# Optimization experiments

Measured on AMD Instinct MI355X. Metric: run time of the kernel, lower is better.

## Reference

```python
import jax, jax.numpy as jnp
import numpy as np

HEADS = 8
DIM_HEAD = 64


def setup_inputs() -> dict:
    key = jax.random.key(0)
    ks = jax.random.split(key, 4)
    B, C, H, W = 1, 256, 64, 64
    inner = HEADS * DIM_HEAD  # 512
    x = jax.random.normal(ks[0], (B, C, H, W), dtype=jnp.float32)
    norm_w = jnp.ones((C,), dtype=jnp.float32)                      # RMSNorm weight (1,C,1,1) flattened
    w_qkv = jax.random.normal(ks[1], (3 * inner, C), dtype=jnp.float32) * 0.02  # 1x1 conv, no bias
    w_out = jax.random.normal(ks[2], (C, inner), dtype=jnp.float32) * 0.02      # 1x1 conv
    b_out = jax.random.normal(ks[3], (C,), dtype=jnp.float32) * 0.02
    return {"x": x, "norm_w": norm_w, "w_qkv": w_qkv, "w_out": w_out, "b_out": b_out}


def reference(x, norm_w, w_qkv, w_out, b_out):
    B, C, H, W = x.shape
    N = H * W
    # RMSNorm: F.normalize over channel dim (L2, eps clamp) * weight * sqrt(C)
    l2 = jnp.sqrt(jnp.sum(x * x, axis=1, keepdims=True))
    xn = x / jnp.maximum(l2, 1e-12) * norm_w[None, :, None, None] * (C ** 0.5)
    # 1x1 conv QKV = channel matmul
    qkv = jnp.einsum('oc,bchw->bohw', w_qkv, xn)  # [B, 3*inner, H, W]
    q, k, v = jnp.split(qkv, 3, axis=1)

    def split_heads(t):
        # 'b (h d) x y -> b h (x y) d'
        return t.reshape(B, HEADS, DIM_HEAD, N).transpose(0, 1, 3, 2)

    q, k, v = map(split_heads, (q, k, v))
    scale = DIM_HEAD ** -0.5
    scores = jnp.einsum('bhnd,bhmd->bhnm', q, k) * scale  # [B,H,N,N]
    attn = jax.nn.softmax(scores, axis=-1)
    out = jnp.einsum('bhnm,bhmd->bhnd', attn, v)
    # 'b h (x y) d -> b (h d) x y'
    out = out.transpose(0, 1, 3, 2).reshape(B, HEADS * DIM_HEAD, H, W)
    # output 1x1 conv + residual (note: residual is the NORMALIZED x, per source)
    return jnp.einsum('ci,bihw->bchw', w_out, out) + b_out[None, :, None, None] + xn
```

## Files before the change

### kernel.cpp

```cpp
#include <hip/hip_runtime.h>


#define NPIX 4096
#define CIN 256
#define INNER 512
#define NHEAD 8
#define DH 64

typedef _Float16 f16;
typedef __attribute__((ext_vector_type(8))) _Float16 f16x8;
typedef __attribute__((ext_vector_type(4))) float f32x4;

static __device__ __forceinline__ f32x4 mfma_f16(f16x8 a, f16x8 b, f32x4 c) {
  return __builtin_amdgcn_mfma_f32_16x16x32_f16(a, b, c, 0, 0, 0);
}

static __device__ __forceinline__ unsigned pk2(float lo, float hi) {
  return __builtin_bit_cast(unsigned, __builtin_amdgcn_cvt_pkrtz(lo, hi));
}

__global__ __launch_bounds__(256) void k_cvt2(const float* __restrict__ a1, int n1,
                                              const float* __restrict__ a2, int n2,
                                              f16* __restrict__ b) {
  int i = blockIdx.x * 256 + threadIdx.x;
  if (i < n1) b[i] = (f16)a1[i];
  else if (i < n1 + n2) b[i] = (f16)a2[i - n1];
}

__global__ __launch_bounds__(256) void k_rmsnorm(const float* __restrict__ x,
                                                 const float* __restrict__ w,
                                                 float* __restrict__ xn,
                                                 f16* __restrict__ xnT) {
  const int pi = threadIdx.x & 15, cs = threadIdx.x >> 4;
  const int p = blockIdx.x * 16 + pi;
  __shared__ float red[16][16];
  float xv[16];
  float ss = 0.f;
#pragma unroll
  for (int i = 0; i < 16; ++i) {
    xv[i] = x[(cs * 16 + i) * NPIX + p];
    ss += xv[i] * xv[i];
  }
  red[cs][pi] = ss;
  __syncthreads();
  float tot = 0.f;
#pragma unroll
  for (int s = 0; s < 16; ++s) tot += red[s][pi];
  float inv = 16.0f / fmaxf(sqrtf(tot), 1e-12f);
  union { f16x8 v[2]; f16 h[16]; } hv;
#pragma unroll
  for (int i = 0; i < 16; ++i) {
    int c = cs * 16 + i;
    float v = xv[i] * inv * w[c];
    xn[c * NPIX + p] = v;
    hv.h[i] = (f16)v;
  }
  *(f16x8*)(xnT + (size_t)p * CIN + cs * 16) = hv.v[0];
  *(f16x8*)(xnT + (size_t)p * CIN + cs * 16 + 8) = hv.v[1];
}

__global__ __launch_bounds__(256) void k_qkv(const f16* __restrict__ wqkv,
                                             const f16* __restrict__ xnT,
                                             f16* __restrict__ qT,
                                             f16* __restrict__ kT,
                                             f16* __restrict__ vv) {
  const int lane = threadIdx.x & 63, wave = threadIdx.x >> 6;
  const int l15 = lane & 15, quad = lane >> 4;
  const int obase = blockIdx.y * 64 + (wave >> 1) * 32;
  const int pbase = blockIdx.x * 128 + (wave & 1) * 64;
  const int sect = blockIdx.y >> 3;
  f32x4 acc[8];
#pragma unroll
  for (int i = 0; i < 8; ++i) acc[i] = (f32x4){0.f, 0.f, 0.f, 0.f};
#pragma unroll
  for (int kc = 0; kc < CIN / 32; ++kc) {
    f16x8 af[2], bfr[4];
#pragma unroll
    for (int oc = 0; oc < 2; ++oc)
      af[oc] = *(const f16x8*)(wqkv + (size_t)(obase + oc * 16 + l15) * CIN + kc * 32 + quad * 8);
#pragma unroll
    for (int pc = 0; pc < 4; ++pc)
      bfr[pc] = *(const f16x8*)(xnT + (size_t)(pbase + pc * 16 + l15) * CIN + kc * 32 + quad * 8);
    if (sect < 2) {
#pragma unroll
      for (int pc = 0; pc < 4; ++pc)
#pragma unroll
        for (int oc = 0; oc < 2; ++oc)
          acc[pc * 2 + oc] = mfma_f16(bfr[pc], af[oc], acc[pc * 2 + oc]);
    } else {
#pragma unroll
      for (int oc = 0; oc < 2; ++oc)
#pragma unroll
        for (int pc = 0; pc < 4; ++pc)
          acc[oc * 4 + pc] = mfma_f16(af[oc], bfr[pc], acc[oc * 4 + pc]);
    }
  }
  if (sect < 2) {
    f16* dst = (sect == 0) ? qT : kT;
    const float sc = (sect == 0) ? 0.18033688f : 1.0f;
    const int head = blockIdx.y & 7;
    const int dd = (wave >> 1) * 32;
#pragma unroll
    for (int pc = 0; pc < 4; ++pc)
#pragma unroll
      for (int oc = 0; oc < 2; ++oc)
#pragma unroll
        for (int r = 0; r < 4; ++r) {
          int p = pbase + pc * 16 + quad * 4 + r;
          dst[((size_t)(head << 12) + p) * DH + dd + oc * 16 + l15] =
              (f16)(acc[pc * 2 + oc][r] * sc);
        }
  } else {
#pragma unroll
    for (int oc = 0; oc < 2; ++oc)
#pragma unroll
      for (int r = 0; r < 4; ++r) {
        int o = obase + oc * 16 + quad * 4 + r - 2 * INNER;
#pragma unroll
        for (int pc = 0; pc < 4; ++pc)
          vv[(size_t)o * NPIX + pbase + pc * 16 + l15] = (f16)acc[oc * 4 + pc][r];
      }
  }
}

__global__ __launch_bounds__(512, 2) void k_attn(const f16* __restrict__ qT,
                                                 const f16* __restrict__ kT,
                                                 const f16* __restrict__ vv,
                                                 f16* __restrict__ Ows) {
  const int head = blockIdx.x & 7;
  const int qb = (blockIdx.x >> 3) * 128;
  const int tid = threadIdx.x;
  const int wave = tid >> 6, lane = tid & 63;
  const int l15 = lane & 15, quad = lane >> 4;

  extern __shared__ float smem[];
  float (*Om)[4][64][17] = reinterpret_cast<float (*)[4][64][17]>(smem);
  float (*Ll)[4][16]     = reinterpret_cast<float (*)[4][16]>(smem + 8 * 4 * 64 * 17);

  f16x8 qf[8][2];
#pragma unroll
  for (int qt = 0; qt < 8; ++qt)
#pragma unroll
    for (int kc = 0; kc < 2; ++kc)
      qf[qt][kc] = *(const f16x8*)(qT + ((size_t)(head << 12) + qb + qt * 16 + l15) * DH + kc * 32 + quad * 8);

  f32x4 o[8][4];
  float ol[8];
#pragma unroll
  for (int qt = 0; qt < 8; ++qt) {
#pragma unroll
    for (int c = 0; c < 4; ++c) o[qt][c] = (f32x4){0.f, 0.f, 0.f, 0.f};
    ol[qt] = 0.f;
  }

  const f16* kbase = kT + (size_t)(head << 12) * DH;
  const f16* vbase = vv + (size_t)(head * DH) * NPIX;
  const int kb0 = wave * (NPIX / 8);
  const int srcA4 = (((quad & 1) << 5) + l15) * 4;
  const int srcB4 = srcA4 + 64;
  const bool hiQuad = quad >= 2;

  for (int it = 0; it < 16; ++it) {
    const int kb = kb0 + it * 32;
    f16x8 kf[2][2];
#pragma unroll
    for (int nc = 0; nc < 2; ++nc)
#pragma unroll
      for (int kc = 0; kc < 2; ++kc)
        kf[nc][kc] = *(const f16x8*)(kbase + (size_t)(kb + nc * 16 + l15) * DH + kc * 32 + quad * 8);
    f16x8 vf[4];
#pragma unroll
    for (int c = 0; c < 4; ++c)
      vf[c] = *(const f16x8*)(vbase + (size_t)(c * 16 + l15) * NPIX + kb + quad * 8);

#define S_QT(QT, S)                                                       \
  do {                                                                    \
    S[0] = mfma_f16(kf[0][0], qf[QT][0], (f32x4){0.f, 0.f, 0.f, 0.f});    \
    S[0] = mfma_f16(kf[0][1], qf[QT][1], S[0]);                           \
    S[1] = mfma_f16(kf[1][0], qf[QT][0], (f32x4){0.f, 0.f, 0.f, 0.f});    \
    S[1] = mfma_f16(kf[1][1], qf[QT][1], S[1]);                           \
  } while (0)

    f32x4 sc[2], sn[2];
    __builtin_amdgcn_s_setprio(1);
    S_QT(0, sc);
    __builtin_amdgcn_s_setprio(0);
#pragma unroll
    for (int qt = 0; qt < 8; ++qt) {
      if (qt < 7) {
        __builtin_amdgcn_s_setprio(1);
        S_QT(qt + 1, sn);
        __builtin_amdgcn_s_setprio(0);
      }
      float p0[4], p1[4];
#pragma unroll
      for (int r = 0; r < 4; ++r) {
        p0[r] = __builtin_amdgcn_exp2f(sc[0][r]);
        p1[r] = __builtin_amdgcn_exp2f(sc[1][r]);
      }
      ol[qt] += ((p0[0] + p0[1]) + (p0[2] + p0[3])) +
                ((p1[0] + p1[1]) + (p1[2] + p1[3]));
      unsigned A0 = pk2(p0[0], p0[1]), B0 = pk2(p0[2], p0[3]);
      unsigned A1 = pk2(p1[0], p1[1]), B1 = pk2(p1[2], p1[3]);
      unsigned As = hiQuad ? A1 : A0;
      unsigned Bs = hiQuad ? B1 : B0;
      union { f16x8 v; unsigned u[4]; } pf;
      pf.u[0] = (unsigned)__builtin_amdgcn_ds_bpermute(srcA4, (int)As);
      pf.u[1] = (unsigned)__builtin_amdgcn_ds_bpermute(srcA4, (int)Bs);
      pf.u[2] = (unsigned)__builtin_amdgcn_ds_bpermute(srcB4, (int)As);
      pf.u[3] = (unsigned)__builtin_amdgcn_ds_bpermute(srcB4, (int)Bs);
      __builtin_amdgcn_s_setprio(1);
#pragma unroll
      for (int c = 0; c < 4; ++c) o[qt][c] = mfma_f16(vf[c], pf.v, o[qt][c]);
      __builtin_amdgcn_s_setprio(0);
      if (qt < 7) { sc[0] = sn[0]; sc[1] = sn[1]; }
    }
#undef S_QT
  }

#pragma unroll
  for (int qt = 0; qt < 8; ++qt) {
    ol[qt] += __shfl_xor(ol[qt], 16);
    ol[qt] += __shfl_xor(ol[qt], 32);
  }

#pragma unroll
  for (int pass = 0; pass < 2; ++pass) {
    if (pass) __syncthreads();
#pragma unroll
    for (int qt2 = 0; qt2 < 4; ++qt2) {
      const int qt = pass * 4 + qt2;
      if (quad == 0) Ll[wave][qt2][l15] = ol[qt];
#pragma unroll
      for (int c = 0; c < 4; ++c)
#pragma unroll
        for (int r = 0; r < 4; ++r)
          Om[wave][qt2][c * 16 + quad * 4 + r][l15] = o[qt][c][r];
    }
    __syncthreads();
    const int d = tid & 63;
    const int mqt = wave >> 1, qh = (wave & 1) * 8;
#pragma unroll
    for (int j = 0; j < 8; ++j) {
      const int q = qh + j;
      float O = 0.f, L = 0.f;
#pragma unroll
      for (int w = 0; w < 8; ++w) {
        O += Om[w][mqt][d][q];
        L += Ll[w][mqt][q];
      }
      Ows[((size_t)(head << 12) + qb + (pass * 4 + mqt) * 16 + q) * DH + d] =
          (f16)(O / L);
    }
  }
}

__global__ __launch_bounds__(256) void k_oproj(const f16* __restrict__ wout,
                                               const f16* __restrict__ Ows,
                                               const float* __restrict__ bout,
                                               const float* __restrict__ xn,
                                               float* __restrict__ out) {
  const int lane = threadIdx.x & 63, wave = threadIdx.x >> 6;
  const int l15 = lane & 15, quad = lane >> 4;
  const int mbase = blockIdx.y * 32 + (wave >> 1) * 16;
  const int pbase = blockIdx.x * 64 + (wave & 1) * 32;
  f32x4 acc[2];
  acc[0] = (f32x4){0.f, 0.f, 0.f, 0.f};
  acc[1] = (f32x4){0.f, 0.f, 0.f, 0.f};
#pragma unroll
  for (int kc = 0; kc < INNER / 32; ++kc) {
    f16x8 af = *(const f16x8*)(wout + (size_t)(mbase + l15) * INNER + kc * 32 + quad * 8);
    int i0 = kc * 32 + quad * 8;
    int head = i0 >> 6, d0 = i0 & 63;
#pragma unroll
    for (int pc = 0; pc < 2; ++pc) {
      f16x8 bfr = *(const f16x8*)(Ows + ((size_t)(head << 12) + pbase + pc * 16 + l15) * DH + d0);
      acc[pc] = mfma_f16(af, bfr, acc[pc]);
    }
  }
#pragma unroll
  for (int pc = 0; pc < 2; ++pc)
#pragma unroll
    for (int r = 0; r < 4; ++r) {
      int c = mbase + quad * 4 + r, p = pbase + pc * 16 + l15;
      out[c * NPIX + p] = acc[pc][r] + bout[c] + xn[c * NPIX + p];
    }
}

extern "C" void kernel_launch(void* const* d_in, const int* in_sizes, int n_in,
                              void* d_out, int out_size, void* d_ws, size_t ws_size,
                              hipStream_t stream) {
  (void)in_sizes; (void)n_in; (void)out_size; (void)ws_size;
  const float* x      = (const float*)d_in[0];
  const float* norm_w = (const float*)d_in[1];
  const float* w_qkv  = (const float*)d_in[2];
  const float* w_out  = (const float*)d_in[3];
  const float* b_out  = (const float*)d_in[4];
  float* out = (float*)d_out;

  char* ws = (char*)d_ws;
  float* xn    = (float*)(ws);
  f16* xnT     = (f16*)(ws + (4u << 20));
  f16* qT      = (f16*)(ws + (6u << 20));
  f16* kT      = (f16*)(ws + (10u << 20));
  f16* vv      = (f16*)(ws + (14u << 20));
  f16* Ows     = (f16*)(ws + (18u << 20));
  f16* wqkv_h  = (f16*)(ws + (22u << 20));
  f16* wout_h  = (f16*)(ws + (22u << 20) + 786432);

  const int n1 = 3 * INNER * CIN, n2 = CIN * INNER;
  hipLaunchKernelGGL(k_cvt2, dim3((n1 + n2 + 255) / 256), dim3(256), 0, stream,
                     w_qkv, n1, w_out, n2, wqkv_h);
  hipLaunchKernelGGL(k_rmsnorm, dim3(NPIX / 16), dim3(256), 0, stream, x, norm_w, xn, xnT);
  hipLaunchKernelGGL(k_qkv, dim3(NPIX / 128, 1536 / 64), dim3(256), 0, stream,
                     wqkv_h, xnT, qT, kT, vv);
  hipLaunchKernelGGL(k_attn, dim3(256), dim3(512), 141312, stream,
                     qT, kT, vv, Ows);
  hipLaunchKernelGGL(k_oproj, dim3(NPIX / 64, CIN / 32), dim3(256), 0, stream,
                     wout_h, Ows, b_out, xn, out);
}
```

Measured before the change: 169.1 us.

## Split attention over keys with LDS-staged K/V tiles and a merge kernel

The attention kernel is restructured: each block now handles 128 queries for one head and one quarter of the keys. K/V tiles are double-buffered in LDS through direct global-to-LDS loads with XOR swizzling, so waves share them instead of each loading K/V from global memory. Partial outputs and row sums go to workspace and a new merge kernel combines them. This drops the large LDS cross-wave reduction and raises the block count for occupancy, at the cost of extra global traffic for the partials and one more launch.

New measurement: 154.8 us. -8.5%, faster.

```diff
diff --git a/kernel.cpp b/kernel.cpp
--- a/kernel.cpp
+++ b/kernel.cpp
@@ -17,6 +17,12 @@
 
 static __device__ __forceinline__ unsigned pk2(float lo, float hi) {
   return __builtin_bit_cast(unsigned, __builtin_amdgcn_cvt_pkrtz(lo, hi));
+}
+
+static __device__ __forceinline__ void gload_lds16(const void* g, void* l) {
+  __builtin_amdgcn_global_load_lds(
+      (const __attribute__((address_space(1))) unsigned*)g,
+      (__attribute__((address_space(3))) unsigned*)l, 16, 0, 0);
 }
 
 __global__ __launch_bounds__(256) void k_cvt2(const float* __restrict__ a1, int n1,
@@ -123,136 +129,171 @@
   }
 }
 
-__global__ __launch_bounds__(512, 2) void k_attn(const f16* __restrict__ qT,
+template <typename PT>
+__global__ __launch_bounds__(256, 4) void k_attn(const f16* __restrict__ qT,
                                                  const f16* __restrict__ kT,
                                                  const f16* __restrict__ vv,
-                                                 f16* __restrict__ Ows) {
-  const int head = blockIdx.x & 7;
-  const int qb = (blockIdx.x >> 3) * 128;
+                                                 PT* __restrict__ Opart,
+                                                 float* __restrict__ Lpart) {
+  const int bid = blockIdx.x;
+  const int head = bid & 7, split = (bid >> 3) & 3, qb = bid >> 5;
   const int tid = threadIdx.x;
   const int wave = tid >> 6, lane = tid & 63;
   const int l15 = lane & 15, quad = lane >> 4;
-
-  extern __shared__ float smem[];
-  float (*Om)[4][64][17] = reinterpret_cast<float (*)[4][64][17]>(smem);
-  float (*Ll)[4][16]     = reinterpret_cast<float (*)[4][16]>(smem + 8 * 4 * 64 * 17);
-
-  f16x8 qf[8][2];
-#pragma unroll
-  for (int qt = 0; qt < 8; ++qt)
+  const int keybase = split * 1024;
+
+  __shared__ f16 KV[2][8192];
+
+  const int qrow = (head << 12) + qb * 128 + wave * 32;
+  f16x8 qf[2][2];
+#pragma unroll
+  for (int qt = 0; qt < 2; ++qt)
 #pragma unroll
     for (int kc = 0; kc < 2; ++kc)
-      qf[qt][kc] = *(const f16x8*)(qT + ((size_t)(head << 12) + qb + qt * 16 + l15) * DH + kc * 32 + quad * 8);
-
-  f32x4 o[8][4];
-  float ol[8];
-#pragma unroll
-  for (int qt = 0; qt < 8; ++qt) {
+      qf[qt][kc] = *(const f16x8*)(qT + (size_t)(qrow + qt * 16 + l15) * DH + kc * 32 + quad * 8);
+
+  f32x4 o[2][4];
+  float ol[2] = {0.f, 0.f};
+#pragma unroll
+  for (int qt = 0; qt < 2; ++qt)
 #pragma unroll
     for (int c = 0; c < 4; ++c) o[qt][c] = (f32x4){0.f, 0.f, 0.f, 0.f};
-    ol[qt] = 0.f;
-  }
-
-  const f16* kbase = kT + (size_t)(head << 12) * DH;
-  const f16* vbase = vv + (size_t)(head * DH) * NPIX;
-  const int kb0 = wave * (NPIX / 8);
+
+  const int sKey8 = lane >> 3;
+  const int sCol = lane & 7;
+  const int rx = l15 & 7;
   const int srcA4 = (((quad & 1) << 5) + l15) * 4;
   const int srcB4 = srcA4 + 64;
   const bool hiQuad = quad >= 2;
 
-  for (int it = 0; it < 16; ++it) {
-    const int kb = kb0 + it * 32;
-    f16x8 kf[2][2];
-#pragma unroll
-    for (int nc = 0; nc < 2; ++nc)
-#pragma unroll
-      for (int kc = 0; kc < 2; ++kc)
-        kf[nc][kc] = *(const f16x8*)(kbase + (size_t)(kb + nc * 16 + l15) * DH + kc * 32 + quad * 8);
-    f16x8 vf[4];
-#pragma unroll
-    for (int c = 0; c < 4; ++c)
-      vf[c] = *(const f16x8*)(vbase + (size_t)(c * 16 + l15) * NPIX + kb + quad * 8);
-
-#define S_QT(QT, S)                                                       \
-  do {                                                                    \
-    S[0] = mfma_f16(kf[0][0], qf[QT][0], (f32x4){0.f, 0.f, 0.f, 0.f});    \
-    S[0] = mfma_f16(kf[0][1], qf[QT][1], S[0]);                           \
-    S[1] = mfma_f16(kf[1][0], qf[QT][0], (f32x4){0.f, 0.f, 0.f, 0.f});    \
-    S[1] = mfma_f16(kf[1][1], qf[QT][1], S[1]);                           \
-  } while (0)
-
-    f32x4 sc[2], sn[2];
-    __builtin_amdgcn_s_setprio(1);
-    S_QT(0, sc);
-    __builtin_amdgcn_s_setprio(0);
-#pragma unroll
-    for (int qt = 0; qt < 8; ++qt) {
-      if (qt < 7) {
-        __builtin_amdgcn_s_setprio(1);
-        S_QT(qt + 1, sn);
-        __builtin_amdgcn_s_setprio(0);
-      }
-      float p0[4], p1[4];
-#pragma unroll
-      for (int r = 0; r < 4; ++r) {
-        p0[r] = __builtin_amdgcn_exp2f(sc[0][r]);
-        p1[r] = __builtin_amdgcn_exp2f(sc[1][r]);
-      }
-      ol[qt] += ((p0[0] + p0[1]) + (p0[2] + p0[3])) +
-                ((p1[0] + p1[1]) + (p1[2] + p1[3]));
-      unsigned A0 = pk2(p0[0], p0[1]), B0 = pk2(p0[2], p0[3]);
-      unsigned A1 = pk2(p1[0], p1[1]), B1 = pk2(p1[2], p1[3]);
-      unsigned As = hiQuad ? A1 : A0;
-      unsigned Bs = hiQuad ? B1 : B0;
-      union { f16x8 v; unsigned u[4]; } pf;
-      pf.u[0] = (unsigned)__builtin_amdgcn_ds_bpermute(srcA4, (int)As);
-      pf.u[1] = (unsigned)__builtin_amdgcn_ds_bpermute(srcA4, (int)Bs);
-      pf.u[2] = (unsigned)__builtin_amdgcn_ds_bpermute(srcB4, (int)As);
-      pf.u[3] = (unsigned)__builtin_amdgcn_ds_bpermute(srcB4, (int)Bs);
-      __builtin_amdgcn_s_setprio(1);
-#pragma unroll
-      for (int c = 0; c < 4; ++c) o[qt][c] = mfma_f16(vf[c], pf.v, o[qt][c]);
-      __builtin_amdgcn_s_setprio(0);
-      if (qt < 7) { sc[0] = sn[0]; sc[1] = sn[1]; }
-    }
-#undef S_QT
-  }
-
-#pragma unroll
-  for (int qt = 0; qt < 8; ++qt) {
+  auto stage = [&](int ch, int b) {
+    const int R0 = wave * 4096;
+#pragma unroll
+    for (int j = 0; j < 4; ++j) {
+      const int Rb = R0 + j * 1024;
+      char* ldst = (char*)(&KV[b][0]) + Rb;
+      if (Rb < 8192) {
+        const int key = (Rb >> 7) + sKey8;
+        const f16* src = kT + ((size_t)(head << 12) + keybase + ch * 64 + key) * DH +
+                         ((sCol ^ (key & 7)) << 3);
+        gload_lds16(src, ldst);
+      } else {
+        const int dd = ((Rb - 8192) >> 7) + sKey8;
+        const f16* src = vv + ((size_t)(head * DH) + dd) * NPIX + keybase + ch * 64 +
+                         ((sCol ^ (dd & 7)) << 3);
+        gload_lds16(src, ldst);
+      }
+    }
+  };
+
+  stage(0, 0);
+  __syncthreads();
+
+  for (int ch = 0; ch < 16; ++ch) {
+    const int b = ch & 1;
+    if (ch < 15) stage(ch + 1, b ^ 1);
+    const f16* Kb = &KV[b][0];
+    const f16* Vb = &KV[b][4096];
+#pragma unroll
+    for (int h = 0; h < 2; ++h) {
+      f16x8 kf[2][2], vf[4];
+#pragma unroll
+      for (int nc = 0; nc < 2; ++nc) {
+        const int key = h * 32 + nc * 16 + l15;
+#pragma unroll
+        for (int kc = 0; kc < 2; ++kc)
+          kf[nc][kc] = *(const f16x8*)(Kb + key * 64 + (((kc * 4 + quad) ^ rx) << 3));
+      }
+#pragma unroll
+      for (int c = 0; c < 4; ++c) {
+        const int dd = c * 16 + l15;
+        vf[c] = *(const f16x8*)(Vb + dd * 64 + (((h * 4 + quad) ^ rx) << 3));
+      }
+#pragma unroll
+      for (int qt = 0; qt < 2; ++qt) {
+        f32x4 s0 = mfma_f16(kf[0][0], qf[qt][0], (f32x4){0.f, 0.f, 0.f, 0.f});
+        s0 = mfma_f16(kf[0][1], qf[qt][1], s0);
+        f32x4 s1 = mfma_f16(kf[1][0], qf[qt][0], (f32x4){0.f, 0.f, 0.f, 0.f});
+        s1 = mfma_f16(kf[1][1], qf[qt][1], s1);
+        float p0[4], p1[4];
+#pragma unroll
+        for (int r = 0; r < 4; ++r) {
+          p0[r] = __builtin_amdgcn_exp2f(s0[r]);
+          p1[r] = __builtin_amdgcn_exp2f(s1[r]);
+        }
+        ol[qt] += ((p0[0] + p0[1]) + (p0[2] + p0[3])) +
+                  ((p1[0] + p1[1]) + (p1[2] + p1[3]));
+        unsigned A0 = pk2(p0[0], p0[1]), B0 = pk2(p0[2], p0[3]);
+        unsigned A1 = pk2(p1[0], p1[1]), B1 = pk2(p1[2], p1[3]);
+        unsigned As = hiQuad ? A1 : A0;
+        unsigned Bs = hiQuad ? B1 : B0;
+        union { f16x8 v; unsigned u[4]; } pf;
+        pf.u[0] = (unsigned)__builtin_amdgcn_ds_bpermute(srcA4, (int)As);
+        pf.u[1] = (unsigned)__builtin_amdgcn_ds_bpermute(srcA4, (int)Bs);
+        pf.u[2] = (unsigned)__builtin_amdgcn_ds_bpermute(srcB4, (int)As);
+        pf.u[3] = (unsigned)__builtin_amdgcn_ds_bpermute(srcB4, (int)Bs);
+#pragma unroll
+        for (int c = 0; c < 4; ++c) o[qt][c] = mfma_f16(vf[c], pf.v, o[qt][c]);
+      }
+    }
+    __syncthreads();
+  }
+
+#pragma unroll
+  for (int qt = 0; qt < 2; ++qt) {
     ol[qt] += __shfl_xor(ol[qt], 16);
     ol[qt] += __shfl_xor(ol[qt], 32);
   }
 
 #pragma unroll
-  for (int pass = 0; pass < 2; ++pass) {
-    if (pass) __syncthreads();
-#pragma unroll
-    for (int qt2 = 0; qt2 < 4; ++qt2) {
-      const int qt = pass * 4 + qt2;
-      if (quad == 0) Ll[wave][qt2][l15] = ol[qt];
-#pragma unroll
-      for (int c = 0; c < 4; ++c)
-#pragma unroll
-        for (int r = 0; r < 4; ++r)
-          Om[wave][qt2][c * 16 + quad * 4 + r][l15] = o[qt][c][r];
-    }
-    __syncthreads();
-    const int d = tid & 63;
-    const int mqt = wave >> 1, qh = (wave & 1) * 8;
-#pragma unroll
-    for (int j = 0; j < 8; ++j) {
-      const int q = qh + j;
-      float O = 0.f, L = 0.f;
-#pragma unroll
-      for (int w = 0; w < 8; ++w) {
-        O += Om[w][mqt][d][q];
-        L += Ll[w][mqt][q];
-      }
-      Ows[((size_t)(head << 12) + qb + (pass * 4 + mqt) * 16 + q) * DH + d] =
-          (f16)(O / L);
-    }
-  }
+  for (int qt = 0; qt < 2; ++qt) {
+#pragma unroll
+    for (int c = 0; c < 4; ++c)
+#pragma unroll
+      for (int r = 0; r < 4; ++r)
+        Opart[((size_t)split * 32768 + qrow + qt * 16 + l15) * 64 + c * 16 + quad * 4 + r] =
+            (PT)o[qt][c][r];
+    if (quad == 0) Lpart[split * 32768 + qrow + qt * 16 + l15] = ol[qt];
+  }
+}
+
+template <typename PT>
+__global__ __launch_bounds__(256) void k_merge(const PT* __restrict__ Opart,
+                                               const float* __restrict__ Lpart,
+                                               f16* __restrict__ Ows) {
+  const int tg = blockIdx.x * 256 + threadIdx.x;
+  const int qi = tg >> 2;
+  const size_t base = (size_t)tg * 16;
+  float acc[16];
+#pragma unroll
+  for (int i = 0; i < 16; ++i) acc[i] = 0.f;
+  float L = 0.f;
+#pragma unroll
+  for (int s = 0; s < 4; ++s) {
+    const PT* p = Opart + (size_t)s * (32768 * 64) + base;
+    if constexpr (sizeof(PT) == 4) {
+      const float4* p4 = (const float4*)p;
+      float4 v0 = p4[0], v1 = p4[1], v2 = p4[2], v3 = p4[3];
+      acc[0] += v0.x; acc[1] += v0.y; acc[2] += v0.z; acc[3] += v0.w;
+      acc[4] += v1.x; acc[5] += v1.y; acc[6] += v1.z; acc[7] += v1.w;
+      acc[8] += v2.x; acc[9] += v2.y; acc[10] += v2.z; acc[11] += v2.w;
+      acc[12] += v3.x; acc[13] += v3.y; acc[14] += v3.z; acc[15] += v3.w;
+    } else {
+      const f16x8* ph = (const f16x8*)p;
+      f16x8 v0 = ph[0], v1 = ph[1];
+#pragma unroll
+      for (int i = 0; i < 8; ++i) {
+        acc[i] += (float)v0[i];
+        acc[8 + i] += (float)v1[i];
+      }
+    }
+    L += Lpart[s * 32768 + qi];
+  }
+  union { f16x8 v[2]; f16 h[16]; } hv;
+#pragma unroll
+  for (int i = 0; i < 16; ++i) hv.h[i] = (f16)(acc[i] / L);
+  *(f16x8*)(Ows + base) = hv.v[0];
+  *(f16x8*)(Ows + base + 8) = hv.v[1];
 }
 
 __global__ __launch_bounds__(256) void k_oproj(const f16* __restrict__ wout,
@@ -290,7 +331,7 @@
 extern "C" void kernel_launch(void* const* d_in, const int* in_sizes, int n_in,
                               void* d_out, int out_size, void* d_ws, size_t ws_size,
                               hipStream_t stream) {
-  (void)in_sizes; (void)n_in; (void)out_size; (void)ws_size;
+  (void)in_sizes; (void)n_in; (void)out_size;
   const float* x      = (const float*)d_in[0];
   const float* norm_w = (const float*)d_in[1];
   const float* w_qkv  = (const float*)d_in[2];
@@ -314,8 +355,25 @@
   hipLaunchKernelGGL(k_rmsnorm, dim3(NPIX / 16), dim3(256), 0, stream, x, norm_w, xn, xnT);
   hipLaunchKernelGGL(k_qkv, dim3(NPIX / 128, 1536 / 64), dim3(256), 0, stream,
                      wqkv_h, xnT, qT, kT, vv);
-  hipLaunchKernelGGL(k_attn, dim3(256), dim3(512), 141312, stream,
-                     qT, kT, vv, Ows);
+
+  const size_t OPLANE = (size_t)32768 * 64;
+  char* pbase = ws + (24u << 20);
+  if (ws_size >= (24u << 20) + OPLANE * 4 * sizeof(float) + 4 * 32768 * sizeof(float)) {
+    float* Op = (float*)pbase;
+    float* Lp = (float*)(pbase + OPLANE * 4 * sizeof(float));
+    hipLaunchKernelGGL((k_attn<float>), dim3(1024), dim3(256), 0, stream,
+                       qT, kT, vv, Op, Lp);
+    hipLaunchKernelGGL((k_merge<float>), dim3(512), dim3(256), 0, stream,
+                       Op, Lp, Ows);
+  } else {
+    f16* Op = (f16*)pbase;
+    float* Lp = (float*)(pbase + OPLANE * 4 * sizeof(f16));
+    hipLaunchKernelGGL((k_attn<f16>), dim3(1024), dim3(256), 0, stream,
+                       qT, kT, vv, Op, Lp);
+    hipLaunchKernelGGL((k_merge<f16>), dim3(512), dim3(256), 0, stream,
+                       Op, Lp, Ows);
+  }
+
   hipLaunchKernelGGL(k_oproj, dim3(NPIX / 64, CIN / 32), dim3(256), 0, stream,
                      wout_h, Ows, b_out, xn, out);
 }
```
